# Kernel tuning notes

Measured on AMD Instinct MI355X. Metric: run time of the kernel, lower is better.

## Reference

```python
import jax, jax.numpy as jnp
import numpy as np

N_NODES = 50000
N_EDGES = 800000
DIMS = [100, 512, 256, 128, 200]  # input -> conv1 -> conv2 -> conv3 -> conv4


def setup_inputs() -> dict:
    key = jax.random.key(0)
    ks = jax.random.split(key, 2 + 4)
    x = jax.random.normal(ks[0], (N_NODES, DIMS[0]), dtype=jnp.float32)
    edge_index = jax.random.randint(ks[1], (2, N_EDGES), 0, N_NODES, dtype=jnp.int64)
    inp = {"x": x, "edge_index": edge_index}
    for i in range(4):
        fan_in = DIMS[i]
        W = jax.random.normal(ks[2 + i], (DIMS[i], DIMS[i + 1]), dtype=jnp.float32) * (1.0 / np.sqrt(fan_in)).astype(np.float32)
        b = jnp.zeros((DIMS[i + 1],), dtype=jnp.float32)
        inp[f"W{i + 1}"] = W
        inp[f"b{i + 1}"] = b
    return inp


def _gcn_layer(x, row, col, norm, W, b, n):
    # PyG GCNConv: linear transform first, then normalized scatter-add, then bias.
    h = x @ W                           # [N, out]
    msg = h[row] * norm[:, None]        # [E+N, out] gather + edge scale
    agg = jax.ops.segment_sum(msg, col, num_segments=n)  # scatter-add to targets
    return agg + b


def reference(x, edge_index, W1, b1, W2, b2, W3, b3, W4, b4):
    n = x.shape[0]
    loop = jnp.arange(n, dtype=edge_index.dtype)
    row = jnp.concatenate([edge_index[0], loop])  # sources (with self-loops)
    col = jnp.concatenate([edge_index[1], loop])  # targets (with self-loops)
    deg = jax.ops.segment_sum(jnp.ones_like(col, dtype=x.dtype), col, num_segments=n)
    dinv = jnp.where(deg > 0, jax.lax.rsqrt(deg), 0.0)
    norm = dinv[row] * dinv[col]  # symmetric D^{-1/2}(A+I)D^{-1/2} edge weights

    out = jax.nn.relu(_gcn_layer(x, row, col, norm, W1, b1, n))
    out = jax.nn.relu(_gcn_layer(out, row, col, norm, W2, b2, n))
    out = jax.nn.relu(_gcn_layer(out, row, col, norm, W3, b3, n))
    out = jax.nn.relu(_gcn_layer(out, row, col, norm, W4, b4, n))
    return jnp.mean(out, axis=0, keepdims=True)  # [1, 200]
```

## Files before the change

kernel.cpp:

```cpp
#include <hip/hip_runtime.h>
#include <hip/hip_bf16.h>


#define NN 50000
#define NE 800000
#define PRANGE (NN / 8)
#define CAP 64

typedef __attribute__((ext_vector_type(8))) _Float16 f16x8;
typedef __attribute__((ext_vector_type(4))) float floatx4;
typedef __attribute__((ext_vector_type(2))) float floatx2;

union U16x8 {
    uint4 u4;
    f16x8 h;
    _Float16 e[8];
};

__device__ __forceinline__ void dec16(const unsigned char* p, float* f) {
    uint4 v = *(const uint4*)p;
    unsigned w[4] = {v.x, v.y, v.z, v.w};
#pragma unroll
    for (int k = 0; k < 4; k++) {
        floatx2 lo = __builtin_amdgcn_cvt_pk_f32_fp8(w[k], false);
        floatx2 hi = __builtin_amdgcn_cvt_pk_f32_fp8(w[k], true);
        f[k * 4 + 0] = lo[0];
        f[k * 4 + 1] = lo[1];
        f[k * 4 + 2] = hi[0];
        f[k * 4 + 3] = hi[1];
    }
}

__device__ __forceinline__ uint4 enc16(const float* f) {
    uint4 r;
    unsigned w;
    w = __builtin_amdgcn_cvt_pk_fp8_f32(f[0], f[1], 0, false);
    w = __builtin_amdgcn_cvt_pk_fp8_f32(f[2], f[3], (int)w, true);
    r.x = w;
    w = __builtin_amdgcn_cvt_pk_fp8_f32(f[4], f[5], 0, false);
    w = __builtin_amdgcn_cvt_pk_fp8_f32(f[6], f[7], (int)w, true);
    r.y = w;
    w = __builtin_amdgcn_cvt_pk_fp8_f32(f[8], f[9], 0, false);
    w = __builtin_amdgcn_cvt_pk_fp8_f32(f[10], f[11], (int)w, true);
    r.z = w;
    w = __builtin_amdgcn_cvt_pk_fp8_f32(f[12], f[13], 0, false);
    w = __builtin_amdgcn_cvt_pk_fp8_f32(f[14], f[15], (int)w, true);
    r.w = w;
    return r;
}

__device__ __forceinline__ uint4 dec8_f16(uint2 v) {
    floatx2 f0 = __builtin_amdgcn_cvt_pk_f32_fp8(v.x, false);
    floatx2 f1 = __builtin_amdgcn_cvt_pk_f32_fp8(v.x, true);
    floatx2 f2 = __builtin_amdgcn_cvt_pk_f32_fp8(v.y, false);
    floatx2 f3 = __builtin_amdgcn_cvt_pk_f32_fp8(v.y, true);
    U16x8 o;
    o.e[0] = (_Float16)f0[0]; o.e[1] = (_Float16)f0[1];
    o.e[2] = (_Float16)f1[0]; o.e[3] = (_Float16)f1[1];
    o.e[4] = (_Float16)f2[0]; o.e[5] = (_Float16)f2[1];
    o.e[6] = (_Float16)f3[0]; o.e[7] = (_Float16)f3[1];
    return o.u4;
}

__global__ __launch_bounds__(256) void zero_kernel(unsigned* __restrict__ fillc,
                                                   float* __restrict__ out) {
    int tid = blockIdx.x * 256 + threadIdx.x;
    if (tid < NN) fillc[tid] = 0u;
    if (blockIdx.x == 0 && threadIdx.x < 200) out[threadIdx.x] = 0.f;
}

__global__ __launch_bounds__(256) void fillcast_kernel(
    const void* __restrict__ ei, unsigned* __restrict__ fillc,
    int* __restrict__ ep, const float* __restrict__ x,
    unsigned char* __restrict__ xb,
    const float* __restrict__ W1, const float* __restrict__ W2,
    const float* __restrict__ W3, const float* __restrict__ W4,
    _Float16* __restrict__ w1t, _Float16* __restrict__ w2t,
    _Float16* __restrict__ w3t, _Float16* __restrict__ w4t) {
    int bx = blockIdx.x, t = threadIdx.x;
    if (bx < 6256) {
        const int part = bx & 7;
        const int lo = part * PRANGE, hi = lo + PRANGE;
        const int group = bx >> 3;
        const int base = (group * 256 + t) * 4;
        __shared__ int nz;
        if (t == 0) nz = 0;
        __syncthreads();
        int dbase = (base <= NE - 4) ? base : (NE - 4);
        unsigned w = ((const unsigned*)ei)[2 * (size_t)dbase + 1];
        if (w) atomicOr(&nz, 1);
        __syncthreads();
        const int f64 = (nz == 0);
        const long long* p64 = (const long long*)ei;
        const int* p32 = (const int*)ei;
#pragma unroll
        for (int i = 0; i < 4; i++) {
            int e = base + i;
            if (e >= NE) break;
            int c = f64 ? (int)p64[NE + e] : p32[NE + e];
            if (c >= lo && c < hi) {
                int idx = (int)atomicAdd(&fillc[c], 1u);
                if (idx < CAP) {
                    int r = f64 ? (int)p64[e] : p32[e];
                    ep[c * CAP + idx] = r;
                }
            }
        }
        return;
    }
    if (bx < 6256 + 1563) {
        int tid = (bx - 6256) * 256 + t;
        int node = tid >> 3, sub = tid & 7;
        if (node >= NN) return;
        int base = sub * 16;
        float f[16];
#pragma unroll
        for (int i = 0; i < 16; i++) {
            int cc = base + i;
            f[i] = (cc < 100) ? x[(size_t)node * 100 + cc] : 0.f;
        }
        *(uint4*)(xb + (size_t)node * 128 + base) = enc16(f);
        return;
    }
    int b = bx - 6256 - 1563;
    const float* W;
    _Float16* Wt;
    int K, N, Kpad, tid;
    if (b < 256)      { W = W1; Wt = w1t; K = 100; N = 512; Kpad = 128; tid = b * 256 + t; }
    else if (b < 768) { W = W2; Wt = w2t; K = 512; N = 256; Kpad = 512; tid = (b - 256) * 256 + t; }
    else if (b < 896) { W = W3; Wt = w3t; K = 256; N = 128; Kpad = 256; tid = (b - 768) * 256 + t; }
    else              { W = W4; Wt = w4t; K = 128; N = 200; Kpad = 128; tid = (b - 896) * 256 + t; }
    int n = tid / Kpad, k = tid - n * Kpad;
    float v = (k < K && n < N) ? W[(size_t)k * N + n] : 0.f;
    Wt[tid] = (_Float16)v;
}

template <int D, int BR, int PS, int SS>
__global__ __launch_bounds__(256) void agg_kernel(
    const unsigned char* __restrict__ H, const int* __restrict__ ep,
    const unsigned* __restrict__ fillc, const float* __restrict__ bias,
    unsigned char* __restrict__ O) {
    constexpr int LPN = D / 16;
    int tid = blockIdx.x * 256 + threadIdx.x;
    int node = tid / LPN;
    int sub = tid % LPN;
    if (node >= NN) return;
    int degt = (int)fillc[node];
    int deg = degt > CAP ? CAP : degt;
    const int s = node * CAP;
    const int e = s + deg;
    float dc = rsqrtf((float)(degt + 1));
    const int base = sub * 16;
    const unsigned char* __restrict__ Hb = H + base;
    float acc[16], t0[16], t1[16];
    dec16(Hb + (size_t)node * D, t0);
    if (SS) {
#pragma unroll
        for (int i = 0; i < 16; i++) acc[i] = t0[i];
        int j = s;
        for (; j + 2 <= e; j += 2) {
            int r0 = ep[j];
            int r1 = ep[j + 1];
            dec16(Hb + (size_t)r0 * D, t0);
            dec16(Hb + (size_t)r1 * D, t1);
#pragma unroll
            for (int i = 0; i < 16; i++) acc[i] += t0[i];
#pragma unroll
            for (int i = 0; i < 16; i++) acc[i] += t1[i];
        }
        if (j < e) {
            int r0 = ep[j];
            dec16(Hb + (size_t)r0 * D, t0);
#pragma unroll
            for (int i = 0; i < 16; i++) acc[i] += t0[i];
        }
#pragma unroll
        for (int i = 0; i < 16; i++) acc[i] *= dc;
    } else {
        float selfw = dc * dc;
#pragma unroll
        for (int i = 0; i < 16; i++) acc[i] = selfw * t0[i];
        int j = s;
        for (; j + 2 <= e; j += 2) {
            int r0 = ep[j];
            int r1 = ep[j + 1];
            float w0 = rsqrtf((float)((int)fillc[r0] + 1)) * dc;
            float w1 = rsqrtf((float)((int)fillc[r1] + 1)) * dc;
            dec16(Hb + (size_t)r0 * D, t0);
            dec16(Hb + (size_t)r1 * D, t1);
#pragma unroll
            for (int i = 0; i < 16; i++) acc[i] = fmaf(w0, t0[i], acc[i]);
#pragma unroll
            for (int i = 0; i < 16; i++) acc[i] = fmaf(w1, t1[i], acc[i]);
        }
        if (j < e) {
            int r0 = ep[j];
            float w0 = rsqrtf((float)((int)fillc[r0] + 1)) * dc;
            dec16(Hb + (size_t)r0 * D, t0);
#pragma unroll
            for (int i = 0; i < 16; i++) acc[i] = fmaf(w0, t0[i], acc[i]);
        }
    }
    if (BR) {
#pragma unroll
        for (int i = 0; i < 16; i++) acc[i] = fmaxf(acc[i] + bias[base + i], 0.f);
    }
    if (PS) {
#pragma unroll
        for (int i = 0; i < 16; i++) acc[i] *= dc;
    }
    *(uint4*)(O + (size_t)node * D + base) = enc16(acc);
}

template <int SS, int EPI>
__global__ __launch_bounds__(256) void aggemm_kernel(
    const unsigned char* __restrict__ H, const int* __restrict__ ep,
    const unsigned* __restrict__ fillc, const float* __restrict__ bias,
    const _Float16* __restrict__ B, unsigned char* __restrict__ Cb,
    float* __restrict__ outmean, int N) {
    __shared__ _Float16 Alds[4][64][36];
    __shared__ _Float16 Bsl[128 * 36];
    __shared__ float red[128];
    const int m0 = blockIdx.x * 64;
    const int t = threadIdx.x;

#pragma unroll
    for (int it = 0; it < 2; ++it) {
        int u = t + it * 256;
        int nl = u >> 3;
        int sub = u & 7;
        int node = m0 + nl;
        int nd = node < NN ? node : NN - 1;
        int degt = (int)fillc[nd];
        int deg = degt > CAP ? CAP : degt;
        const int s = nd * CAP;
        const int e = s + deg;
        float dc = rsqrtf((float)(degt + 1));
        const int base = sub * 16;
        const unsigned char* __restrict__ Hb = H + base;
        float acc[16], t0[16], t1[16];
        dec16(Hb + (size_t)nd * 128, t0);
        if (SS) {
#pragma unroll
            for (int i = 0; i < 16; i++) acc[i] = t0[i];
            int j = s;
            for (; j + 2 <= e; j += 2) {
                int r0 = ep[j];
                int r1 = ep[j + 1];
                dec16(Hb + (size_t)r0 * 128, t0);
                dec16(Hb + (size_t)r1 * 128, t1);
#pragma unroll
                for (int i = 0; i < 16; i++) acc[i] += t0[i];
#pragma unroll
                for (int i = 0; i < 16; i++) acc[i] += t1[i];
            }
            if (j < e) {
                int r0 = ep[j];
                dec16(Hb + (size_t)r0 * 128, t0);
#pragma unroll
                for (int i = 0; i < 16; i++) acc[i] += t0[i];
            }
#pragma unroll
            for (int i = 0; i < 16; i++) acc[i] *= dc;
        } else {
            float selfw = dc * dc;
#pragma unroll
            for (int i = 0; i < 16; i++) acc[i] = selfw * t0[i];
            int j = s;
            for (; j + 2 <= e; j += 2) {
                int r0 = ep[j];
                int r1 = ep[j + 1];
                float w0 = rsqrtf((float)((int)fillc[r0] + 1)) * dc;
                float w1 = rsqrtf((float)((int)fillc[r1] + 1)) * dc;
                dec16(Hb + (size_t)r0 * 128, t0);
                dec16(Hb + (size_t)r1 * 128, t1);
#pragma unroll
                for (int i = 0; i < 16; i++) acc[i] = fmaf(w0, t0[i], acc[i]);
#pragma unroll
                for (int i = 0; i < 16; i++) acc[i] = fmaf(w1, t1[i], acc[i]);
            }
            if (j < e) {
                int r0 = ep[j];
                float w0 = rsqrtf((float)((int)fillc[r0] + 1)) * dc;
                dec16(Hb + (size_t)r0 * 128, t0);
#pragma unroll
                for (int i = 0; i < 16; i++) acc[i] = fmaf(w0, t0[i], acc[i]);
            }
        }
        U16x8 lo, hi;
#pragma unroll
        for (int i = 0; i < 8; i++) { lo.e[i] = (_Float16)acc[i]; hi.e[i] = (_Float16)acc[8 + i]; }
        _Float16* dst = &Alds[sub >> 1][nl][(sub & 1) * 16];
        *(uint4*)dst = lo.u4;
        *(uint4*)(dst + 8) = hi.u4;
    }
    __syncthreads();

    const int lane = t & 63, w = t >> 6;
    const int wm = (w >> 1) * 32, wn = (w & 1) * 64;
    const int r16 = lane & 15, quad = lane >> 4;
    const int rb0 = t >> 2, kb0 = (t & 3) * 8;
    const int rb1 = (t + 256) >> 2;
    const int NT = (N + 127) / 128;

    for (int nt = 0; nt < NT; ++nt) {
        const int n0 = nt * 128;
        const _Float16* Bp0 = B + (size_t)(n0 + rb0) * 128 + kb0;
        const _Float16* Bp1 = B + (size_t)(n0 + rb1) * 128 + kb0;
        floatx4 acc[2][4];
        const floatx4 fz = {0.f, 0.f, 0.f, 0.f};
#pragma unroll
        for (int i = 0; i < 2; i++)
#pragma unroll
            for (int j = 0; j < 4; j++) acc[i][j] = fz;
        uint4 bpf0 = *(const uint4*)Bp0;
        uint4 bpf1 = *(const uint4*)Bp1;
#pragma unroll
        for (int kc = 0; kc < 128; kc += 32) {
            __syncthreads();
            *(uint4*)(Bsl + rb0 * 36 + kb0) = bpf0;
            *(uint4*)(Bsl + rb1 * 36 + kb0) = bpf1;
            __syncthreads();
            if (kc + 32 < 128) {
                bpf0 = *(const uint4*)(Bp0 + kc + 32);
                bpf1 = *(const uint4*)(Bp1 + kc + 32);
            }
            f16x8 af[2], bf[4];
#pragma unroll
            for (int i = 0; i < 2; i++)
                af[i] = *(const f16x8*)(&Alds[kc >> 5][wm + i * 16 + r16][quad * 8]);
#pragma unroll
            for (int j = 0; j < 4; j++)
                bf[j] = *(const f16x8*)(Bsl + (wn + j * 16 + r16) * 36 + quad * 8);
#pragma unroll
            for (int i = 0; i < 2; i++)
#pragma unroll
                for (int j = 0; j < 4; j++)
                    acc[i][j] = __builtin_amdgcn_mfma_f32_16x16x32_f16(af[i], bf[j], acc[i][j], 0, 0, 0);
        }
        if (EPI == 2) {
            __syncthreads();
            if (t < 128) red[t] = 0.f;
            __syncthreads();
#pragma unroll
            for (int j = 0; j < 4; j++) {
                int col = n0 + wn + j * 16 + r16;
                float s = 0.f;
                if (col < N) {
                    float bv = bias[col];
#pragma unroll
                    for (int i = 0; i < 2; i++) {
                        int mbase = m0 + wm + i * 16 + quad * 4;
#pragma unroll
                        for (int r = 0; r < 4; r++)
                            if (mbase + r < NN) s += fmaxf(acc[i][j][r] + bv, 0.f);
                    }
                }
                atomicAdd(&red[wn + j * 16 + r16], s);
            }
            __syncthreads();
            if (t < 128) {
                int col = n0 + t;
                if (col < N) atomicAdd(outmean + col, red[t] * (1.0f / (float)NN));
            }
        } else {
#pragma unroll
            for (int i = 0; i < 2; i++) {
                int mbase = m0 + wm + i * 16 + quad * 4;
#pragma unroll
                for (int r = 0; r < 4; r++) {
                    int m = mbase + r;
                    if (m >= NN) continue;
#pragma unroll
                    for (int j = 0; j < 4; j++) {
                        int col = n0 + wn + j * 16 + r16;
                        float v = acc[i][j][r];
                        v = fmaxf(v + bias[col], 0.f);
                        unsigned pk = __builtin_amdgcn_cvt_pk_fp8_f32(v, v, 0, false);
                        Cb[(size_t)m * N + col] = (unsigned char)(pk & 0xffu);
                    }
                }
            }
        }
    }
}

template <int EPI, int PS>
__global__ __launch_bounds__(256) void gemm_kernel(
    const unsigned char* __restrict__ A, const _Float16* __restrict__ B,
    const float* __restrict__ bias, const unsigned* __restrict__ fillc,
    unsigned char* __restrict__ Cb, float* __restrict__ outmean,
    int M, int K, int N) {
    __shared__ _Float16 Asl[128 * 36];
    __shared__ _Float16 Bsl[128 * 36];
    const int m0 = blockIdx.y * 128;
    const int n0 = blockIdx.x * 128;
    const int t = threadIdx.x;
    const int lane = t & 63, w = t >> 6;
    const int wm = (w >> 1) * 64, wn = (w & 1) * 64;
    const int r16 = lane & 15, quad = lane >> 4;

    const int arow = t >> 1, ac16 = (t & 1) * 16;
    int gma = m0 + arow; if (gma > M - 1) gma = M - 1;
    const unsigned char* Aptr = A + (size_t)gma * K + ac16;
    const int rb0 = t >> 2, kb0 = (t & 3) * 8;
    const int rb1 = (t + 256) >> 2;
    const _Float16* Bptr0 = B + (size_t)(n0 + rb0) * K + kb0;
    const _Float16* Bptr1 = B + (size_t)(n0 + rb1) * K + kb0;

    floatx4 acc[4][4];
    const floatx4 fz = {0.f, 0.f, 0.f, 0.f};
#pragma unroll
    for (int i = 0; i < 4; i++)
#pragma unroll
        for (int j = 0; j < 4; j++) acc[i][j] = fz;

    uint4 apf = *(const uint4*)Aptr;
    uint4 bpf0 = *(const uint4*)Bptr0;
    uint4 bpf1 = *(const uint4*)Bptr1;

    for (int kc = 0; kc < K; kc += 32) {
        __syncthreads();
        uint2 alo = {apf.x, apf.y}, ahi = {apf.z, apf.w};
        *(uint4*)(Asl + arow * 36 + ac16) = dec8_f16(alo);
        *(uint4*)(Asl + arow * 36 + ac16 + 8) = dec8_f16(ahi);
        *(uint4*)(Bsl + rb0 * 36 + kb0) = bpf0;
        *(uint4*)(Bsl + rb1 * 36 + kb0) = bpf1;
        __syncthreads();
        if (kc + 32 < K) {
            apf = *(const uint4*)(Aptr + kc + 32);
            bpf0 = *(const uint4*)(Bptr0 + kc + 32);
            bpf1 = *(const uint4*)(Bptr1 + kc + 32);
        }
        f16x8 af[4], bf[4];
#pragma unroll
        for (int i = 0; i < 4; i++)
            af[i] = *(const f16x8*)(Asl + (wm + i * 16 + r16) * 36 + quad * 8);
#pragma unroll
        for (int j = 0; j < 4; j++)
            bf[j] = *(const f16x8*)(Bsl + (wn + j * 16 + r16) * 36 + quad * 8);
#pragma unroll
        for (int i = 0; i < 4; i++)
#pragma unroll
            for (int j = 0; j < 4; j++)
                acc[i][j] = __builtin_amdgcn_mfma_f32_16x16x32_f16(af[i], bf[j], acc[i][j], 0, 0, 0);
    }

#pragma unroll
    for (int i = 0; i < 4; i++) {
        int mbase = m0 + wm + i * 16 + quad * 4;
#pragma unroll
        for (int r = 0; r < 4; r++) {
            int m = mbase + r;
            if (m >= M) continue;
            float dsc = 1.f;
            if (PS) dsc = rsqrtf((float)((int)fillc[m] + 1));
#pragma unroll
            for (int j = 0; j < 4; j++) {
                int col = n0 + wn + j * 16 + r16;
                float v = acc[i][j][r];
                if (EPI == 1) v = fmaxf(v + bias[col], 0.f);
                if (PS) v *= dsc;
                unsigned pk = __builtin_amdgcn_cvt_pk_fp8_f32(v, v, 0, false);
                Cb[(size_t)m * N + col] = (unsigned char)(pk & 0xffu);
            }
        }
    }
}

extern "C" void kernel_launch(void* const* d_in, const int* in_sizes, int n_in,
                              void* d_out, int out_size, void* d_ws, size_t ws_size,
                              hipStream_t stream) {
    const float* x  = (const float*)d_in[0];
    const void*  ei = d_in[1];
    const float* W1 = (const float*)d_in[2];
    const float* b1 = (const float*)d_in[3];
    const float* W2 = (const float*)d_in[4];
    const float* b2 = (const float*)d_in[5];
    const float* W3 = (const float*)d_in[6];
    const float* b3 = (const float*)d_in[7];
    const float* W4 = (const float*)d_in[8];
    const float* b4 = (const float*)d_in[9];
    float* out = (float*)d_out;

    char* ws = (char*)d_ws;
    size_t o = 0;
    auto alloc = [&](size_t bytes) -> void* {
        void* p = ws + o;
        o += (bytes + 255) & ~(size_t)255;
        return p;
    };
    unsigned* fillc = (unsigned*)alloc((size_t)NN * 4);
    int*      ep    = (int*)alloc((size_t)NN * CAP * 4);
    _Float16* w1t = (_Float16*)alloc((size_t)512 * 128 * 2);
    _Float16* w2t = (_Float16*)alloc((size_t)256 * 512 * 2);
    _Float16* w3t = (_Float16*)alloc((size_t)128 * 256 * 2);
    _Float16* w4t = (_Float16*)alloc((size_t)256 * 128 * 2);
    unsigned char* xb  = (unsigned char*)alloc((size_t)NN * 128);
    unsigned char* H1b = (unsigned char*)alloc((size_t)NN * 512);
    unsigned char* t2b = (unsigned char*)alloc((size_t)NN * 256);
    unsigned char* H2b = (unsigned char*)alloc((size_t)NN * 256);
    unsigned char* t3b = (unsigned char*)alloc((size_t)NN * 128);
    unsigned char* h3b = (unsigned char*)alloc((size_t)NN * 128);

    zero_kernel<<<196, 256, 0, stream>>>(fillc, out);
    fillcast_kernel<<<6256 + 1563 + 1024, 256, 0, stream>>>(
        ei, fillc, ep, x, xb, W1, W2, W3, W4, w1t, w2t, w3t, w4t);

    const int MB64 = (NN + 63) / 64;
    const int MB128 = (NN + 127) / 128;
    const int AB128 = (NN * 8 + 255) / 256;
    const int AB256 = (NN * 16 + 255) / 256;

    aggemm_kernel<0, 1><<<MB64, 256, 0, stream>>>(xb, ep, fillc, b1, w1t, H1b, nullptr, 512);
    gemm_kernel<0, 1><<<dim3(2, MB128), 256, 0, stream>>>(H1b, w2t, nullptr, fillc, t2b, nullptr, NN, 512, 256);
    agg_kernel<256, 1, 0, 1><<<AB256, 256, 0, stream>>>(t2b, ep, fillc, b2, H2b);
    gemm_kernel<0, 1><<<dim3(1, MB128), 256, 0, stream>>>(H2b, w3t, nullptr, fillc, t3b, nullptr, NN, 256, 128);
    agg_kernel<128, 1, 1, 1><<<AB128, 256, 0, stream>>>(t3b, ep, fillc, b3, h3b);
    aggemm_kernel<1, 2><<<MB64, 256, 0, stream>>>(h3b, ep, fillc, b4, w4t, nullptr, out, 200);
}
```

Measured before the change: 320.3 us.

## Double aggemm block to 512 threads, splitting N tiles across two warp groups

```diff
diff --git a/kernel.cpp b/kernel.cpp
--- a/kernel.cpp
+++ b/kernel.cpp
@@ -213,22 +213,21 @@
 }
 
 template <int SS, int EPI>
-__global__ __launch_bounds__(256) void aggemm_kernel(
+__global__ __launch_bounds__(512) void aggemm_kernel(
     const unsigned char* __restrict__ H, const int* __restrict__ ep,
     const unsigned* __restrict__ fillc, const float* __restrict__ bias,
     const _Float16* __restrict__ B, unsigned char* __restrict__ Cb,
     float* __restrict__ outmean, int N) {
-    __shared__ _Float16 Alds[4][64][36];
-    __shared__ _Float16 Bsl[128 * 36];
-    __shared__ float red[128];
+    constexpr int SUBT = 64 * 36 + 32;
+    __shared__ _Float16 Alds[4 * SUBT];
+    __shared__ _Float16 Bsl[2][128 * 36];
+    __shared__ float red[2][128];
     const int m0 = blockIdx.x * 64;
     const int t = threadIdx.x;
 
-#pragma unroll
-    for (int it = 0; it < 2; ++it) {
-        int u = t + it * 256;
-        int nl = u >> 3;
-        int sub = u & 7;
+    {
+        const int nl = t >> 3;
+        const int sub = t & 7;
         int node = m0 + nl;
         int nd = node < NN ? node : NN - 1;
         int degt = (int)fillc[nd];
@@ -290,20 +289,21 @@
         U16x8 lo, hi;
 #pragma unroll
         for (int i = 0; i < 8; i++) { lo.e[i] = (_Float16)acc[i]; hi.e[i] = (_Float16)acc[8 + i]; }
-        _Float16* dst = &Alds[sub >> 1][nl][(sub & 1) * 16];
+        _Float16* dst = Alds + (sub >> 1) * SUBT + nl * 36 + (sub & 1) * 16;
         *(uint4*)dst = lo.u4;
         *(uint4*)(dst + 8) = hi.u4;
     }
-    __syncthreads();
-
-    const int lane = t & 63, w = t >> 6;
+
+    const int g = t >> 8;
+    const int tl = t & 255;
+    const int lane = tl & 63, w = tl >> 6;
     const int wm = (w >> 1) * 32, wn = (w & 1) * 64;
     const int r16 = lane & 15, quad = lane >> 4;
-    const int rb0 = t >> 2, kb0 = (t & 3) * 8;
-    const int rb1 = (t + 256) >> 2;
+    const int rb0 = tl >> 2, kb0 = (tl & 3) * 8;
+    const int rb1 = (tl + 256) >> 2;
     const int NT = (N + 127) / 128;
 
-    for (int nt = 0; nt < NT; ++nt) {
+    for (int nt = g; nt < NT; nt += 2) {
         const int n0 = nt * 128;
         const _Float16* Bp0 = B + (size_t)(n0 + rb0) * 128 + kb0;
         const _Float16* Bp1 = B + (size_t)(n0 + rb1) * 128 + kb0;
@@ -318,8 +318,8 @@
 #pragma unroll
         for (int kc = 0; kc < 128; kc += 32) {
             __syncthreads();
-            *(uint4*)(Bsl + rb0 * 36 + kb0) = bpf0;
-            *(uint4*)(Bsl + rb1 * 36 + kb0) = bpf1;
+            *(uint4*)(Bsl[g] + rb0 * 36 + kb0) = bpf0;
+            *(uint4*)(Bsl[g] + rb1 * 36 + kb0) = bpf1;
             __syncthreads();
             if (kc + 32 < 128) {
                 bpf0 = *(const uint4*)(Bp0 + kc + 32);
@@ -328,10 +328,10 @@
             f16x8 af[2], bf[4];
 #pragma unroll
             for (int i = 0; i < 2; i++)
-                af[i] = *(const f16x8*)(&Alds[kc >> 5][wm + i * 16 + r16][quad * 8]);
+                af[i] = *(const f16x8*)(Alds + (kc >> 5) * SUBT + (wm + i * 16 + r16) * 36 + quad * 8);
 #pragma unroll
             for (int j = 0; j < 4; j++)
-                bf[j] = *(const f16x8*)(Bsl + (wn + j * 16 + r16) * 36 + quad * 8);
+                bf[j] = *(const f16x8*)(Bsl[g] + (wn + j * 16 + r16) * 36 + quad * 8);
 #pragma unroll
             for (int i = 0; i < 2; i++)
 #pragma unroll
@@ -340,7 +340,7 @@
         }
         if (EPI == 2) {
             __syncthreads();
-            if (t < 128) red[t] = 0.f;
+            if (tl < 128) red[g][tl] = 0.f;
             __syncthreads();
 #pragma unroll
             for (int j = 0; j < 4; j++) {
@@ -356,12 +356,12 @@
                             if (mbase + r < NN) s += fmaxf(acc[i][j][r] + bv, 0.f);
                     }
                 }
-                atomicAdd(&red[wn + j * 16 + r16], s);
+                atomicAdd(&red[g][wn + j * 16 + r16], s);
             }
             __syncthreads();
-            if (t < 128) {
-                int col = n0 + t;
-                if (col < N) atomicAdd(outmean + col, red[t] * (1.0f / (float)NN));
+            if (tl < 128) {
+                int col = n0 + tl;
+                if (col < N) atomicAdd(outmean + col, red[g][tl] * (1.0f / (float)NN));
             }
         } else {
 #pragma unroll
@@ -512,10 +512,10 @@
     const int AB128 = (NN * 8 + 255) / 256;
     const int AB256 = (NN * 16 + 255) / 256;
 
-    aggemm_kernel<0, 1><<<MB64, 256, 0, stream>>>(xb, ep, fillc, b1, w1t, H1b, nullptr, 512);
+    aggemm_kernel<0, 1><<<MB64, 512, 0, stream>>>(xb, ep, fillc, b1, w1t, H1b, nullptr, 512);
     gemm_kernel<0, 1><<<dim3(2, MB128), 256, 0, stream>>>(H1b, w2t, nullptr, fillc, t2b, nullptr, NN, 512, 256);
     agg_kernel<256, 1, 0, 1><<<AB256, 256, 0, stream>>>(t2b, ep, fillc, b2, H2b);
     gemm_kernel<0, 1><<<dim3(1, MB128), 256, 0, stream>>>(H2b, w3t, nullptr, fillc, t3b, nullptr, NN, 256, 128);
     agg_kernel<128, 1, 1, 1><<<AB128, 256, 0, stream>>>(t3b, ep, fillc, b3, h3b);
-    aggemm_kernel<1, 2><<<MB64, 256, 0, stream>>>(h3b, ep, fillc, b4, w4t, nullptr, out, 200);
-}
+    aggemm_kernel<1, 2><<<MB64, 512, 0, stream>>>(h3b, ep, fillc, b4, w4t, nullptr, out, 200);
+}
```

Result: no change. 317.4 us (-0.9%).
